# Optimization experiments

Hardware: AMD Instinct MI355X
Metric: run time of the kernel (lower is better)

Reference implementation:

```python
import jax, jax.numpy as jnp
import numpy as np

IN_CHS = 128
NUM_HEADS = 4
WIN = 7
N = WIN * WIN            # 49 tokens per window
QKDIM = 128              # ceil(in_chs/num_groups/num_heads)*num_heads
HEAD_DIM = QKDIM // NUM_HEADS
SCALE = HEAD_DIM ** -0.5
B = 4096                 # batch * num_windows


def _relative_position_index(win_h, win_w):
    coords = np.stack(np.meshgrid(np.arange(win_h), np.arange(win_w), indexing='ij'))  # [2,h,w]
    cf = coords.reshape(2, -1)                      # [2, N]
    rc = (cf[:, :, None] - cf[:, None, :]).transpose(1, 2, 0).astype(np.int64)  # [N,N,2]
    rc[:, :, 0] += win_h - 1
    rc[:, :, 1] += win_w - 1
    rc[:, :, 0] *= 2 * win_w - 1
    return rc.sum(-1)                               # [N, N]


def setup_inputs() -> dict:
    key = jax.random.key(0)
    ks = jax.random.split(key, 8)
    x = jax.random.normal(ks[0], (B, N, IN_CHS), dtype=jnp.float32)
    qk_w = jax.random.normal(ks[1], (2 * QKDIM, IN_CHS), dtype=jnp.float32) * 0.02
    qk_b = jnp.zeros((2 * QKDIM,), dtype=jnp.float32)
    v_w = jax.random.normal(ks[2], (IN_CHS, IN_CHS), dtype=jnp.float32) * 0.02
    v_b = jnp.zeros((IN_CHS,), dtype=jnp.float32)
    proj_w = jax.random.normal(ks[3], (IN_CHS, IN_CHS), dtype=jnp.float32) * 0.02
    proj_b = jnp.zeros((IN_CHS,), dtype=jnp.float32)
    bias_table = jax.random.normal(ks[4], ((2 * WIN - 1) * (2 * WIN - 1), NUM_HEADS), dtype=jnp.float32) * 0.02
    rel_idx = jnp.asarray(_relative_position_index(WIN, WIN))  # [N,N] int64
    return {"x": x, "qk_w": qk_w, "qk_b": qk_b, "v_w": v_w, "v_b": v_b,
            "proj_w": proj_w, "proj_b": proj_b, "bias_table": bias_table,
            "rel_idx": rel_idx}


def reference(x, qk_w, qk_b, v_w, v_b, proj_w, proj_b, bias_table, rel_idx):
    Bn, Nn, C = x.shape
    # fused q/k projection: [B,N,2*qkdim] -> q,k each [B,H,N,d]
    qk = (x @ qk_w.T + qk_b).reshape(Bn, Nn, 2, NUM_HEADS, HEAD_DIM)
    q = qk[:, :, 0].transpose(0, 2, 1, 3)
    k = qk[:, :, 1].transpose(0, 2, 1, 3)
    v = (x @ v_w.T + v_b).reshape(Bn, Nn, NUM_HEADS, -1).transpose(0, 2, 1, 3)
    # windowed QK^T with gathered relative-position bias
    attn = jnp.einsum('bhnd,bhmd->bhnm', q * SCALE, k)
    bias = bias_table[rel_idx.reshape(-1)].reshape(Nn, Nn, NUM_HEADS).transpose(2, 0, 1)
    attn = jax.nn.softmax(attn + bias[None], axis=-1)
    out = jnp.einsum('bhnm,bhmd->bhnd', attn, v).transpose(0, 2, 1, 3).reshape(Bn, Nn, -1)
    return out @ proj_w.T + proj_b
```

## Files before the change

### kernel.cpp

```cpp
#include <hip/hip_runtime.h>
#include <hip/hip_bf16.h>

typedef __attribute__((ext_vector_type(8))) __bf16 bf16x8;
typedef __attribute__((ext_vector_type(4))) short short4v;
typedef __attribute__((ext_vector_type(4))) float f32x4;

#define MFMA(a,b,c) __builtin_amdgcn_mfma_f32_16x16x32_bf16((a),(b),(c),0,0,0)
#define MFMA16(a,b,c) __builtin_amdgcn_mfma_f32_16x16x16bf16_1k((a),(b),(c),0,0,0)

#define XB 0u
#define QB 16384u
#define KB 32768u

static __device__ __forceinline__ unsigned short f2u(float x) {
  return __builtin_bit_cast(unsigned short, static_cast<__bf16>(x));
}
static __device__ __forceinline__ unsigned long long pack4(float a, float b, float c, float d) {
  union { __bf16 h[4]; unsigned long long u; } z;
  z.h[0] = static_cast<__bf16>(a);
  z.h[1] = static_cast<__bf16>(b);
  z.h[2] = static_cast<__bf16>(c);
  z.h[3] = static_cast<__bf16>(d);
  return z.u;
}
static __device__ __forceinline__ unsigned long long pack4v(f32x4 v) {
  return pack4(v[0], v[1], v[2], v[3]);
}
static __device__ __forceinline__ short4v pack4s(float a, float b, float c, float d) {
  union { __bf16 h[4]; short4v s; } z;
  z.h[0] = static_cast<__bf16>(a);
  z.h[1] = static_cast<__bf16>(b);
  z.h[2] = static_cast<__bf16>(c);
  z.h[3] = static_cast<__bf16>(d);
  return z.s;
}
static __device__ __forceinline__ unsigned sw256(unsigned row, unsigned colb) {
  return (row << 8) + (colb ^ ((row & 7u) << 4));
}
static __device__ __forceinline__ unsigned sw128(unsigned row, unsigned colb) {
  return (row << 7) + (colb ^ ((row & 7u) << 4));
}

__global__ void rsa_prep(const float* __restrict__ qk_w, const float* __restrict__ v_w,
                         const float* __restrict__ proj_w, const float* __restrict__ bias_table,
                         unsigned short* __restrict__ wqk, unsigned short* __restrict__ wv,
                         unsigned short* __restrict__ wp, float* __restrict__ biasNN) {
  const float QSCALE = 0.17677669529663687f * 1.4426950408889634f;
  const float LOG2E = 1.4426950408889634f;
  int t = blockIdx.x * blockDim.x + threadIdx.x;
  int stride = gridDim.x * blockDim.x;
  for (int i = t; i < 256 * 128; i += stride) {
    float v = qk_w[i];
    if (i < 128 * 128) v *= QSCALE;
    wqk[i] = f2u(v);
  }
  for (int i = t; i < 128 * 128; i += stride) wv[i] = f2u(v_w[i]);
  for (int i = t; i < 128 * 128; i += stride) wp[i] = f2u(proj_w[i]);
  for (int i = t; i < 4 * 64 * 64; i += stride) {
    int h = i >> 12, r = (i >> 6) & 63, m = i & 63;
    float v = -1e9f;
    if (r < 49 && m < 49) {
      int ri = r / 7, rj = r - ri * 7, mi = m / 7, mj = m - mi * 7;
      int rel = (ri - mi + 6) * 13 + (rj - mj + 6);
      v = bias_table[rel * 4 + h];
    }
    biasNN[i] = v * LOG2E;
  }
}

__global__ __launch_bounds__(512, 6) void rsa_main(
    const float* __restrict__ x, const float* __restrict__ qk_bias,
    const float* __restrict__ v_bias, const float* __restrict__ proj_bias,
    const unsigned short* __restrict__ wqk, const unsigned short* __restrict__ wv,
    const unsigned short* __restrict__ wp, const float* __restrict__ biasNN,
    float* __restrict__ out) {
  __shared__ __align__(16) unsigned char LDS[49152];
  const int tid = threadIdx.x;
  const int w = tid >> 6;
  const int lane = tid & 63;
  const int c = lane & 15;
  const int g = lane >> 4;
  const int b = blockIdx.x;
  const int h = w >> 1;
  const int rt0 = (w & 1) * 2;
  const float QBSCALE = 0.17677669529663687f * 1.4426950408889634f;

  {
    const f32x4* xp = reinterpret_cast<const f32x4*>(x + (size_t)b * 6272);
    for (int i = tid; i < 1568; i += 512) {
      f32x4 v = xp[i];
      unsigned row = (unsigned)i >> 5, c4 = (unsigned)i & 31u;
      *reinterpret_cast<unsigned long long*>(LDS + XB + sw256(row, c4 * 8)) = pack4v(v);
    }
    for (int i = tid; i < 480; i += 512) {
      unsigned row = 49 + ((unsigned)i >> 5), c4 = (unsigned)i & 31u;
      *reinterpret_cast<unsigned long long*>(LDS + XB + sw256(row, c4 * 8)) = 0ull;
    }
  }
  __syncthreads();

  __builtin_amdgcn_s_setprio(1);
#pragma unroll
  for (int mi = 0; mi < 2; ++mi) {
    const int mt = w + 8 * mi;
    bf16x8 a[4];
    const unsigned short* wrow = wqk + (mt * 16 + c) * 128 + g * 8;
#pragma unroll
    for (int ks = 0; ks < 4; ++ks) a[ks] = *reinterpret_cast<const bf16x8*>(wrow + ks * 32);
    f32x4 bias4 = *reinterpret_cast<const f32x4*>(qk_bias + mt * 16 + g * 4);
    if (mi == 0) { bias4[0] *= QBSCALE; bias4[1] *= QBSCALE; bias4[2] *= QBSCALE; bias4[3] *= QBSCALE; }
    f32x4 acc[4];
#pragma unroll
    for (int nt = 0; nt < 4; ++nt) acc[nt] = bias4;
#pragma unroll
    for (int ks = 0; ks < 4; ++ks) {
#pragma unroll
      for (int nt = 0; nt < 4; ++nt) {
        bf16x8 bf = *reinterpret_cast<const bf16x8*>(LDS + XB + sw256(nt * 16 + c, (ks * 32 + g * 8) * 2));
        acc[nt] = MFMA(a[ks], bf, acc[nt]);
      }
    }
    const unsigned base = (mi == 0) ? QB : KB;
    const unsigned colb = ((mt & 7) * 16 + g * 4) * 2;
#pragma unroll
    for (int nt = 0; nt < 4; ++nt)
      *reinterpret_cast<unsigned long long*>(LDS + base + sw256(nt * 16 + c, colb)) = pack4v(acc[nt]);
  }

  f32x4 vacc[4];
  {
    const float vb = v_bias[w * 16 + c];
    bf16x8 bw[4];
    const unsigned short* wrow = wv + (w * 16 + c) * 128 + g * 8;
#pragma unroll
    for (int ks = 0; ks < 4; ++ks) bw[ks] = *reinterpret_cast<const bf16x8*>(wrow + ks * 32);
#pragma unroll
    for (int mt = 0; mt < 4; ++mt) vacc[mt] = f32x4{vb, vb, vb, vb};
#pragma unroll
    for (int ks = 0; ks < 4; ++ks) {
#pragma unroll
      for (int mt = 0; mt < 4; ++mt) {
        bf16x8 af = *reinterpret_cast<const bf16x8*>(LDS + XB + sw256(mt * 16 + c, (ks * 32 + g * 8) * 2));
        vacc[mt] = MFMA(af, bw[ks], vacc[mt]);
      }
    }
  }
  __builtin_amdgcn_s_setprio(0);
  __syncthreads();

#pragma unroll
  for (int mt = 0; mt < 4; ++mt)
    *reinterpret_cast<unsigned long long*>(LDS + XB + sw128(w * 16 + c, (mt * 16 + g * 4) * 2)) =
        pack4v(vacc[mt]);

  short4v pk[2][4];
#pragma unroll
  for (int r2 = 0; r2 < 2; ++r2) {
    f32x4 bbr[4];
    {
      const float* bp = biasNN + ((h * 64 + (rt0 + r2) * 16 + c) << 6);
#pragma unroll
      for (int mt = 0; mt < 4; ++mt)
        bbr[mt] = *reinterpret_cast<const f32x4*>(bp + mt * 16 + g * 4);
    }
    bf16x8 qf = *reinterpret_cast<const bf16x8*>(LDS + QB + sw256((rt0 + r2) * 16 + c, h * 64 + g * 16));
    f32x4 s[4];
    __builtin_amdgcn_s_setprio(1);
#pragma unroll
    for (int mt = 0; mt < 4; ++mt) {
      bf16x8 kf = *reinterpret_cast<const bf16x8*>(LDS + KB + sw256(mt * 16 + c, h * 64 + g * 16));
      s[mt] = MFMA(kf, qf, bbr[mt]);
    }
    __builtin_amdgcn_s_setprio(0);
    float v[16];
#pragma unroll
    for (int mt = 0; mt < 4; ++mt) {
#pragma unroll
      for (int j = 0; j < 4; ++j) v[mt * 4 + j] = exp2f(s[mt][j]);
    }
    float p0 = (v[0] + v[1]) + (v[2] + v[3]);
    float p1 = (v[4] + v[5]) + (v[6] + v[7]);
    float p2 = (v[8] + v[9]) + (v[10] + v[11]);
    float p3 = (v[12] + v[13]) + (v[14] + v[15]);
    float sum = (p0 + p1) + (p2 + p3);
    sum += __shfl_xor(sum, 16);
    sum += __shfl_xor(sum, 32);
    const float inv = __builtin_amdgcn_rcpf(sum);
#pragma unroll
    for (int mt = 0; mt < 4; ++mt)
      pk[r2][mt] = pack4s(v[mt * 4] * inv, v[mt * 4 + 1] * inv,
                          v[mt * 4 + 2] * inv, v[mt * 4 + 3] * inv);
  }
  __syncthreads();

  f32x4 od[2][2];
  {
    short4v vfrag[2][4];
#pragma unroll
    for (int ct2 = 0; ct2 < 2; ++ct2)
#pragma unroll
      for (int ks = 0; ks < 4; ++ks)
        vfrag[ct2][ks] = *reinterpret_cast<const short4v*>(
            LDS + XB + sw128((h * 2 + ct2) * 16 + c, (ks * 16 + g * 4) * 2));
#pragma unroll
    for (int ct2 = 0; ct2 < 2; ++ct2)
#pragma unroll
      for (int r2 = 0; r2 < 2; ++r2) od[ct2][r2] = f32x4{0.f, 0.f, 0.f, 0.f};
    __builtin_amdgcn_s_setprio(1);
#pragma unroll
    for (int ks = 0; ks < 4; ++ks)
#pragma unroll
      for (int ct2 = 0; ct2 < 2; ++ct2)
#pragma unroll
        for (int r2 = 0; r2 < 2; ++r2)
          od[ct2][r2] = MFMA16(vfrag[ct2][ks], pk[r2][ks], od[ct2][r2]);
    __builtin_amdgcn_s_setprio(0);
  }

  bf16x8 ap[4];
  {
    const unsigned short* wrow = wp + (w * 16 + c) * 128 + g * 8;
#pragma unroll
    for (int ks = 0; ks < 4; ++ks) ap[ks] = *reinterpret_cast<const bf16x8*>(wrow + ks * 32);
  }
  f32x4 pb4 = *reinterpret_cast<const f32x4*>(proj_bias + w * 16 + g * 4);

#pragma unroll
  for (int ct2 = 0; ct2 < 2; ++ct2)
#pragma unroll
    for (int r2 = 0; r2 < 2; ++r2) {
      const int r = (rt0 + r2) * 16 + c;
      *reinterpret_cast<unsigned long long*>(
          LDS + QB + sw256(r, ((h * 2 + ct2) * 16 + g * 4) * 2)) = pack4v(od[ct2][r2]);
    }
  __syncthreads();

  {
    f32x4 acc[4];
#pragma unroll
    for (int nt = 0; nt < 4; ++nt) acc[nt] = pb4;
    __builtin_amdgcn_s_setprio(1);
#pragma unroll
    for (int ks = 0; ks < 4; ++ks) {
#pragma unroll
      for (int nt = 0; nt < 4; ++nt) {
        bf16x8 bf = *reinterpret_cast<const bf16x8*>(LDS + QB + sw256(nt * 16 + c, (ks * 32 + g * 8) * 2));
        acc[nt] = MFMA(ap[ks], bf, acc[nt]);
      }
    }
    __builtin_amdgcn_s_setprio(0);
#pragma unroll
    for (int nt = 0; nt < 4; ++nt) {
      const int tok = nt * 16 + c;
      if (tok < 49) {
        *reinterpret_cast<f32x4*>(out + ((size_t)b * 49 + tok) * 128 + w * 16 + g * 4) = acc[nt];
      }
    }
  }
}

extern "C" void kernel_launch(void* const* d_in, const int* in_sizes, int n_in,
                              void* d_out, int out_size, void* d_ws, size_t ws_size,
                              hipStream_t stream) {
  const float* x          = (const float*)d_in[0];
  const float* qk_w       = (const float*)d_in[1];
  const float* qk_b       = (const float*)d_in[2];
  const float* v_w        = (const float*)d_in[3];
  const float* v_b        = (const float*)d_in[4];
  const float* proj_w     = (const float*)d_in[5];
  const float* proj_b     = (const float*)d_in[6];
  const float* bias_table = (const float*)d_in[7];
  float* out = (float*)d_out;

  unsigned short* wqk = (unsigned short*)d_ws;
  unsigned short* wv  = wqk + 256 * 128;
  unsigned short* wp  = wv + 128 * 128;
  float* biasNN = (float*)((char*)d_ws + 131072);

  const int B = in_sizes[0] / (49 * 128);

  rsa_prep<<<dim3(128), dim3(512), 0, stream>>>(qk_w, v_w, proj_w, bias_table, wqk, wv, wp, biasNN);
  rsa_main<<<dim3(B), dim3(512), 0, stream>>>(x, qk_b, v_b, proj_b, wqk, wv, wp, biasNN, out);
}
```

Baseline: 120.2 us.

## Assign one attention head per wave in 256-thread blocks to drop barriers

Shrinks the block from 8 to 4 waves and gives each wave one whole head: its Q/K column tiles, its V channels, all row tiles of the softmax, and two output column tiles. V is written to a separate LDS region, so each wave only reads data it produced itself. That lets two block-wide barriers (between the projections, the softmax and PV) be removed. The trade-off is a larger per-block LDS footprint (64KB) and fewer waves per CU, which reduces latency hiding and puts more work on each wave.

```diff
diff --git a/kernel.cpp b/kernel.cpp
--- a/kernel.cpp
+++ b/kernel.cpp
@@ -11,6 +11,7 @@
 #define XB 0u
 #define QB 16384u
 #define KB 32768u
+#define VT 49152u
 
 static __device__ __forceinline__ unsigned short f2u(float x) {
   return __builtin_bit_cast(unsigned short, static_cast<__bf16>(x));
@@ -68,31 +69,29 @@
   }
 }
 
-__global__ __launch_bounds__(512, 6) void rsa_main(
+__global__ __launch_bounds__(256, 2) void rsa_main(
     const float* __restrict__ x, const float* __restrict__ qk_bias,
     const float* __restrict__ v_bias, const float* __restrict__ proj_bias,
     const unsigned short* __restrict__ wqk, const unsigned short* __restrict__ wv,
     const unsigned short* __restrict__ wp, const float* __restrict__ biasNN,
     float* __restrict__ out) {
-  __shared__ __align__(16) unsigned char LDS[49152];
+  __shared__ __align__(16) unsigned char LDS[65536];
   const int tid = threadIdx.x;
   const int w = tid >> 6;
   const int lane = tid & 63;
   const int c = lane & 15;
   const int g = lane >> 4;
   const int b = blockIdx.x;
-  const int h = w >> 1;
-  const int rt0 = (w & 1) * 2;
   const float QBSCALE = 0.17677669529663687f * 1.4426950408889634f;
 
   {
     const f32x4* xp = reinterpret_cast<const f32x4*>(x + (size_t)b * 6272);
-    for (int i = tid; i < 1568; i += 512) {
+    for (int i = tid; i < 1568; i += 256) {
       f32x4 v = xp[i];
       unsigned row = (unsigned)i >> 5, c4 = (unsigned)i & 31u;
       *reinterpret_cast<unsigned long long*>(LDS + XB + sw256(row, c4 * 8)) = pack4v(v);
     }
-    for (int i = tid; i < 480; i += 512) {
+    for (int i = tid; i < 480; i += 256) {
       unsigned row = 49 + ((unsigned)i >> 5), c4 = (unsigned)i & 31u;
       *reinterpret_cast<unsigned long long*>(LDS + XB + sw256(row, c4 * 8)) = 0ull;
     }
@@ -101,14 +100,14 @@
 
   __builtin_amdgcn_s_setprio(1);
 #pragma unroll
-  for (int mi = 0; mi < 2; ++mi) {
-    const int mt = w + 8 * mi;
+  for (int mi = 0; mi < 4; ++mi) {
+    const int mt = (mi < 2) ? (2 * w + mi) : (6 + 2 * w + mi);
     bf16x8 a[4];
     const unsigned short* wrow = wqk + (mt * 16 + c) * 128 + g * 8;
 #pragma unroll
     for (int ks = 0; ks < 4; ++ks) a[ks] = *reinterpret_cast<const bf16x8*>(wrow + ks * 32);
     f32x4 bias4 = *reinterpret_cast<const f32x4*>(qk_bias + mt * 16 + g * 4);
-    if (mi == 0) { bias4[0] *= QBSCALE; bias4[1] *= QBSCALE; bias4[2] *= QBSCALE; bias4[3] *= QBSCALE; }
+    if (mi < 2) { bias4[0] *= QBSCALE; bias4[1] *= QBSCALE; bias4[2] *= QBSCALE; bias4[3] *= QBSCALE; }
     f32x4 acc[4];
 #pragma unroll
     for (int nt = 0; nt < 4; ++nt) acc[nt] = bias4;
@@ -120,55 +119,55 @@
         acc[nt] = MFMA(a[ks], bf, acc[nt]);
       }
     }
-    const unsigned base = (mi == 0) ? QB : KB;
+    const unsigned base = (mi < 2) ? QB : KB;
     const unsigned colb = ((mt & 7) * 16 + g * 4) * 2;
 #pragma unroll
     for (int nt = 0; nt < 4; ++nt)
       *reinterpret_cast<unsigned long long*>(LDS + base + sw256(nt * 16 + c, colb)) = pack4v(acc[nt]);
   }
 
-  f32x4 vacc[4];
-  {
-    const float vb = v_bias[w * 16 + c];
+#pragma unroll
+  for (int ci = 0; ci < 2; ++ci) {
+    const int ch = w * 32 + ci * 16 + c;
+    const float vb = v_bias[ch];
     bf16x8 bw[4];
-    const unsigned short* wrow = wv + (w * 16 + c) * 128 + g * 8;
+    const unsigned short* wrow = wv + ch * 128 + g * 8;
 #pragma unroll
     for (int ks = 0; ks < 4; ++ks) bw[ks] = *reinterpret_cast<const bf16x8*>(wrow + ks * 32);
-#pragma unroll
-    for (int mt = 0; mt < 4; ++mt) vacc[mt] = f32x4{vb, vb, vb, vb};
+    f32x4 acc[4];
+#pragma unroll
+    for (int mt = 0; mt < 4; ++mt) acc[mt] = f32x4{vb, vb, vb, vb};
 #pragma unroll
     for (int ks = 0; ks < 4; ++ks) {
 #pragma unroll
       for (int mt = 0; mt < 4; ++mt) {
         bf16x8 af = *reinterpret_cast<const bf16x8*>(LDS + XB + sw256(mt * 16 + c, (ks * 32 + g * 8) * 2));
-        vacc[mt] = MFMA(af, bw[ks], vacc[mt]);
-      }
-    }
+        acc[mt] = MFMA(af, bw[ks], acc[mt]);
+      }
+    }
+#pragma unroll
+    for (int mt = 0; mt < 4; ++mt)
+      *reinterpret_cast<unsigned long long*>(LDS + VT + sw128(ch, (mt * 16 + g * 4) * 2)) =
+          pack4v(acc[mt]);
   }
   __builtin_amdgcn_s_setprio(0);
-  __syncthreads();
-
-#pragma unroll
-  for (int mt = 0; mt < 4; ++mt)
-    *reinterpret_cast<unsigned long long*>(LDS + XB + sw128(w * 16 + c, (mt * 16 + g * 4) * 2)) =
-        pack4v(vacc[mt]);
-
-  short4v pk[2][4];
-#pragma unroll
-  for (int r2 = 0; r2 < 2; ++r2) {
+
+  short4v pk[4][4];
+#pragma unroll
+  for (int rt = 0; rt < 4; ++rt) {
     f32x4 bbr[4];
     {
-      const float* bp = biasNN + ((h * 64 + (rt0 + r2) * 16 + c) << 6);
+      const float* bp = biasNN + ((w * 64 + rt * 16 + c) << 6);
 #pragma unroll
       for (int mt = 0; mt < 4; ++mt)
         bbr[mt] = *reinterpret_cast<const f32x4*>(bp + mt * 16 + g * 4);
     }
-    bf16x8 qf = *reinterpret_cast<const bf16x8*>(LDS + QB + sw256((rt0 + r2) * 16 + c, h * 64 + g * 16));
+    bf16x8 qf = *reinterpret_cast<const bf16x8*>(LDS + QB + sw256(rt * 16 + c, w * 64 + g * 16));
     f32x4 s[4];
     __builtin_amdgcn_s_setprio(1);
 #pragma unroll
     for (int mt = 0; mt < 4; ++mt) {
-      bf16x8 kf = *reinterpret_cast<const bf16x8*>(LDS + KB + sw256(mt * 16 + c, h * 64 + g * 16));
+      bf16x8 kf = *reinterpret_cast<const bf16x8*>(LDS + KB + sw256(mt * 16 + c, w * 64 + g * 16));
       s[mt] = MFMA(kf, qf, bbr[mt]);
     }
     __builtin_amdgcn_s_setprio(0);
@@ -188,12 +187,11 @@
     const float inv = __builtin_amdgcn_rcpf(sum);
 #pragma unroll
     for (int mt = 0; mt < 4; ++mt)
-      pk[r2][mt] = pack4s(v[mt * 4] * inv, v[mt * 4 + 1] * inv,
+      pk[rt][mt] = pack4s(v[mt * 4] * inv, v[mt * 4 + 1] * inv,
                           v[mt * 4 + 2] * inv, v[mt * 4 + 3] * inv);
   }
-  __syncthreads();
-
-  f32x4 od[2][2];
+
+  f32x4 od[2][4];
   {
     short4v vfrag[2][4];
 #pragma unroll
@@ -201,45 +199,44 @@
 #pragma unroll
       for (int ks = 0; ks < 4; ++ks)
         vfrag[ct2][ks] = *reinterpret_cast<const short4v*>(
-            LDS + XB + sw128((h * 2 + ct2) * 16 + c, (ks * 16 + g * 4) * 2));
+            LDS + VT + sw128((w * 2 + ct2) * 16 + c, (ks * 16 + g * 4) * 2));
 #pragma unroll
     for (int ct2 = 0; ct2 < 2; ++ct2)
 #pragma unroll
-      for (int r2 = 0; r2 < 2; ++r2) od[ct2][r2] = f32x4{0.f, 0.f, 0.f, 0.f};
+      for (int rt = 0; rt < 4; ++rt) od[ct2][rt] = f32x4{0.f, 0.f, 0.f, 0.f};
     __builtin_amdgcn_s_setprio(1);
 #pragma unroll
     for (int ks = 0; ks < 4; ++ks)
 #pragma unroll
       for (int ct2 = 0; ct2 < 2; ++ct2)
 #pragma unroll
-        for (int r2 = 0; r2 < 2; ++r2)
-          od[ct2][r2] = MFMA16(vfrag[ct2][ks], pk[r2][ks], od[ct2][r2]);
+        for (int rt = 0; rt < 4; ++rt)
+          od[ct2][rt] = MFMA16(vfrag[ct2][ks], pk[rt][ks], od[ct2][rt]);
     __builtin_amdgcn_s_setprio(0);
   }
 
-  bf16x8 ap[4];
-  {
-    const unsigned short* wrow = wp + (w * 16 + c) * 128 + g * 8;
+#pragma unroll
+  for (int ct2 = 0; ct2 < 2; ++ct2)
+#pragma unroll
+    for (int rt = 0; rt < 4; ++rt) {
+      const int r = rt * 16 + c;
+      *reinterpret_cast<unsigned long long*>(
+          LDS + QB + sw256(r, ((w * 2 + ct2) * 16 + g * 4) * 2)) = pack4v(od[ct2][rt]);
+    }
+  __syncthreads();
+
+  __builtin_amdgcn_s_setprio(1);
+#pragma unroll
+  for (int u = 0; u < 2; ++u) {
+    const int ct = 2 * w + u;
+    bf16x8 ap[4];
+    const unsigned short* wrow = wp + (ct * 16 + c) * 128 + g * 8;
 #pragma unroll
     for (int ks = 0; ks < 4; ++ks) ap[ks] = *reinterpret_cast<const bf16x8*>(wrow + ks * 32);
-  }
-  f32x4 pb4 = *reinterpret_cast<const f32x4*>(proj_bias + w * 16 + g * 4);
-
-#pragma unroll
-  for (int ct2 = 0; ct2 < 2; ++ct2)
-#pragma unroll
-    for (int r2 = 0; r2 < 2; ++r2) {
-      const int r = (rt0 + r2) * 16 + c;
-      *reinterpret_cast<unsigned long long*>(
-          LDS + QB + sw256(r, ((h * 2 + ct2) * 16 + g * 4) * 2)) = pack4v(od[ct2][r2]);
-    }
-  __syncthreads();
-
-  {
+    f32x4 pb4 = *reinterpret_cast<const f32x4*>(proj_bias + ct * 16 + g * 4);
     f32x4 acc[4];
 #pragma unroll
     for (int nt = 0; nt < 4; ++nt) acc[nt] = pb4;
-    __builtin_amdgcn_s_setprio(1);
 #pragma unroll
     for (int ks = 0; ks < 4; ++ks) {
 #pragma unroll
@@ -248,15 +245,15 @@
         acc[nt] = MFMA(ap[ks], bf, acc[nt]);
       }
     }
-    __builtin_amdgcn_s_setprio(0);
 #pragma unroll
     for (int nt = 0; nt < 4; ++nt) {
       const int tok = nt * 16 + c;
       if (tok < 49) {
-        *reinterpret_cast<f32x4*>(out + ((size_t)b * 49 + tok) * 128 + w * 16 + g * 4) = acc[nt];
-      }
-    }
-  }
+        *reinterpret_cast<f32x4*>(out + ((size_t)b * 49 + tok) * 128 + ct * 16 + g * 4) = acc[nt];
+      }
+    }
+  }
+  __builtin_amdgcn_s_setprio(0);
 }
 
 extern "C" void kernel_launch(void* const* d_in, const int* in_sizes, int n_in,
@@ -280,5 +277,5 @@
   const int B = in_sizes[0] / (49 * 128);
 
   rsa_prep<<<dim3(128), dim3(512), 0, stream>>>(qk_w, v_w, proj_w, bias_table, wqk, wv, wp, biasNN);
-  rsa_main<<<dim3(B), dim3(512), 0, stream>>>(x, qk_b, v_b, proj_b, wqk, wv, wp, biasNN, out);
-}
+  rsa_main<<<dim3(B), dim3(256), 0, stream>>>(x, qk_b, v_b, proj_b, wqk, wv, wp, biasNN, out);
+}
```

Result: slower. 125.5 us (+4.4%).
